# Performance work log

Hardware: AMD Instinct MI355X
Metric: run time of the kernel (lower is better)

The kernel has to match this reference:

```python
import jax, jax.numpy as jnp
import numpy as np

SH_C0 = 0.28209479177387814
SH_C1 = 0.4886025119029199
SH_C2 = (1.0925484305920792, -1.0925484305920792, 0.31539156525252005, -1.0925484305920792, 0.5462742152960396)
SH_C3 = (-0.5900435899266435, 2.890611442640554, -0.4570457994644658, 0.3731763325901154, -0.4570457994644658, 1.445305721320277, -0.5900435899266435)

BG = 128  # gaussians per compositing block


def quat_to_rot(q):
    # q: [N,4] normalized quaternion (w,x,y,z) -> [N,3,3]
    w, x, y, z = q[:, 0], q[:, 1], q[:, 2], q[:, 3]
    R = jnp.stack([
        1 - 2 * (y * y + z * z), 2 * (x * y - w * z), 2 * (x * z + w * y),
        2 * (x * y + w * z), 1 - 2 * (x * x + z * z), 2 * (y * z - w * x),
        2 * (x * z - w * y), 2 * (y * z + w * x), 1 - 2 * (x * x + y * y)],
        axis=-1)
    return R.reshape(-1, 3, 3)


def eval_sh(sh, d):
    # sh: [N,16,3] degree-3 SH coeffs; d: [N,3] unit view dirs -> [N,3] rgb
    x, y, z = d[:, 0:1], d[:, 1:2], d[:, 2:3]
    xx, yy, zz = x * x, y * y, z * z
    xy, yz, xz = x * y, y * z, x * z
    res = SH_C0 * sh[:, 0]
    res = res - SH_C1 * y * sh[:, 1] + SH_C1 * z * sh[:, 2] - SH_C1 * x * sh[:, 3]
    res = (res + SH_C2[0] * xy * sh[:, 4] + SH_C2[1] * yz * sh[:, 5]
           + SH_C2[2] * (2 * zz - xx - yy) * sh[:, 6]
           + SH_C2[3] * xz * sh[:, 7] + SH_C2[4] * (xx - yy) * sh[:, 8])
    res = (res + SH_C3[0] * y * (3 * xx - yy) * sh[:, 9] + SH_C3[1] * xy * z * sh[:, 10]
           + SH_C3[2] * y * (4 * zz - xx - yy) * sh[:, 11]
           + SH_C3[3] * z * (2 * zz - 3 * xx - 3 * yy) * sh[:, 12]
           + SH_C3[4] * x * (4 * zz - xx - yy) * sh[:, 13]
           + SH_C3[5] * z * (xx - yy) * sh[:, 14] + SH_C3[6] * x * (xx - 3 * yy) * sh[:, 15])
    return res


def gs_forward(pws, shs, alphas_raw, scales_raw, rots_raw, us, Rcw, tcw, intr, height, width):
    fx, fy, cx, cy = intr[0], intr[1], intr[2], intr[3]
    N = pws.shape[0]
    HW = height * width

    # activations (GSModel.forward)
    alphas = jax.nn.sigmoid(alphas_raw[:, 0])          # [N]
    scales = jnp.exp(scales_raw)                       # [N,3]
    rots = rots_raw / jnp.linalg.norm(rots_raw, axis=1, keepdims=True)

    # gsc.project
    pcs = pws @ Rcw.T + tcw                            # [N,3] camera frame
    depth = pcs[:, 2]
    zs = jnp.where(depth > 0.2, depth, 1.0)            # safe divide for culled pts
    u = jnp.stack([fx * pcs[:, 0] / zs + cx, fy * pcs[:, 1] / zs + cy], axis=-1)
    # the `us` input is a grad-capture dummy; forward value comes from projection
    u = u + us - jax.lax.stop_gradient(us)

    # gsc.computeCov3D: Cov3d = (R S)(R S)^T
    R = quat_to_rot(rots)
    M = R * scales[:, None, :]
    cov3d = M @ jnp.swapaxes(M, 1, 2)                  # [N,3,3]

    # gsc.computeCov2D: cov2d = J W Cov3d W^T J^T + 0.3 I
    tanfx = width / (2.0 * fx)
    tanfy = height / (2.0 * fy)
    tx = jnp.clip(pcs[:, 0] / zs, -1.3 * tanfx, 1.3 * tanfx) * zs
    ty = jnp.clip(pcs[:, 1] / zs, -1.3 * tanfy, 1.3 * tanfy) * zs
    zero = jnp.zeros_like(zs)
    J = jnp.stack([
        fx / zs, zero, -fx * tx / (zs * zs),
        zero, fy / zs, -fy * ty / (zs * zs)], axis=-1).reshape(N, 2, 3)
    T = jnp.einsum('nij,jk->nik', J, Rcw)              # [N,2,3]
    cov2d = jnp.einsum('nij,njk,nlk->nil', T, cov3d, T)
    cov2d = cov2d + 0.3 * jnp.eye(2, dtype=cov2d.dtype)
    a, b, c = cov2d[:, 0, 0], cov2d[:, 0, 1], cov2d[:, 1, 1]
    det = a * c - b * b
    valid = (depth > 0.2) & (det > 0)
    det_s = jnp.where(valid, det, 1.0)

    # gsc.inverseCov2D: conic + screen-space radius (areas)
    cinv = jnp.stack([c / det_s, -b / det_s, a / det_s], axis=-1)  # [N,3]
    mid = 0.5 * (a + c)
    lam = mid + jnp.sqrt(jnp.maximum(mid * mid - det, 0.1))
    radius = jnp.where(valid, jnp.ceil(3.0 * jnp.sqrt(lam)), 0.0)
    areas = jnp.stack([radius, radius], axis=-1)       # [N,2]

    # gsc.sh2Color
    twc = -Rcw.T @ tcw
    dirs = pws - twc
    dirs = dirs / jnp.linalg.norm(dirs, axis=1, keepdims=True)
    colors = jnp.maximum(eval_sh(shs.reshape(N, 16, 3), dirs) + 0.5, 0.0)  # [N,3]

    # gsc.splat: depth-sorted front-to-back alpha compositing over all pixels
    order = jnp.argsort(depth)
    nb = N // BG
    u_s = u[order].reshape(nb, BG, 2)
    cinv_s = cinv[order].reshape(nb, BG, 3)
    al_s = alphas[order].reshape(nb, BG)
    col_s = colors[order].reshape(nb, BG, 3)
    val_s = valid[order].reshape(nb, BG)

    ys, xs = jnp.meshgrid(jnp.arange(height, dtype=jnp.float32),
                          jnp.arange(width, dtype=jnp.float32), indexing='ij')
    px = xs.ravel()
    py = ys.ravel()

    @jax.checkpoint
    def body(carry, blk):
        logT, acc = carry                              # [HW], [3,HW]
        ub, cb, ab, colb, vb = blk
        dx = px[None, :] - ub[:, 0:1]                  # [BG,HW]
        dy = py[None, :] - ub[:, 1:2]
        power = -0.5 * (cb[:, 0:1] * dx * dx + cb[:, 2:3] * dy * dy) - cb[:, 1:2] * dx * dy
        alp = jnp.minimum(0.99, ab[:, None] * jnp.exp(power))
        alp = jnp.where((power <= 0) & (alp >= 1.0 / 255.0) & vb[:, None], alp, 0.0)
        l1m = jnp.log1p(-alp)
        cs = jnp.cumsum(l1m, axis=0)
        logT_i = logT[None, :] + jnp.concatenate(
            [jnp.zeros((1, HW), l1m.dtype), cs[:-1]], axis=0)  # exclusive transmittance
        Ti = jnp.exp(logT_i)
        w = jnp.where(Ti > 1e-4, alp * Ti, 0.0)        # early-termination at tau<1e-4
        acc = acc + jnp.einsum('gp,gc->cp', w, colb)
        return (logT + cs[-1], acc), None

    init = (jnp.zeros(HW, dtype=jnp.float32), jnp.zeros((3, HW), dtype=jnp.float32))
    (_, acc), _ = jax.lax.scan(body, init, (u_s, cinv_s, al_s, col_s, val_s))
    image = acc.reshape(3, height, width)
    return image, areas


def setup_inputs() -> dict:
    key = jax.random.key(0)
    ks = jax.random.split(key, 6)
    N, H, W = 8192, 256, 256
    pws = jax.random.normal(ks[0], (N, 3), jnp.float32) * 2.0 + jnp.array([0.0, 0.0, 6.0])
    shs = jax.random.normal(ks[1], (N, 48), jnp.float32) * 0.3
    alphas_raw = jax.random.normal(ks[2], (N, 1), jnp.float32)
    scales_raw = jax.random.normal(ks[3], (N, 3), jnp.float32) * 0.3 - 3.0
    rots_raw = jax.random.normal(ks[4], (N, 4), jnp.float32)
    us = jnp.zeros((N, 2), jnp.float32)
    Rcw = jnp.eye(3, dtype=jnp.float32)
    tcw = jnp.zeros((3,), jnp.float32)
    intr = jnp.array([400.0, 400.0, 128.0, 128.0], jnp.float32)  # fx, fy, cx, cy
    return {"pws": pws, "shs": shs, "alphas_raw": alphas_raw, "scales_raw": scales_raw,
            "rots_raw": rots_raw, "us": us, "Rcw": Rcw, "tcw": tcw, "intr": intr,
            "height": H, "width": W}


def reference(pws, shs, alphas_raw, scales_raw, rots_raw, us, Rcw, tcw, intr, height, width):
    return gs_forward(pws, shs, alphas_raw, scales_raw, rots_raw, us, Rcw, tcw, intr, height, width)
```

## Files before the change

kernel.cpp:

```cpp
#include <hip/hip_runtime.h>

__global__ __launch_bounds__(64) void k_pre(
    const float* __restrict__ pws, const float* __restrict__ shs,
    const float* __restrict__ alphas_raw, const float* __restrict__ scales_raw,
    const float* __restrict__ rots_raw, const float* __restrict__ Rcw,
    const float* __restrict__ tcw, const float* __restrict__ intr,
    int N, int W, int H, float* __restrict__ areas,
    unsigned long long* __restrict__ keys, unsigned* __restrict__ rank,
    float* __restrict__ P)
{
    int i = blockIdx.x * 64 + threadIdx.x;
    if (i >= N) return;
    rank[i] = 0u;

    float R00=Rcw[0],R01=Rcw[1],R02=Rcw[2];
    float R10=Rcw[3],R11=Rcw[4],R12=Rcw[5];
    float R20=Rcw[6],R21=Rcw[7],R22=Rcw[8];
    float t0=tcw[0],t1=tcw[1],t2=tcw[2];
    float fx=intr[0],fy=intr[1],cx=intr[2],cy=intr[3];

    float pwx=pws[i*3+0], pwy=pws[i*3+1], pwz=pws[i*3+2];
    float pcx = R00*pwx + R01*pwy + R02*pwz + t0;
    float pcy = R10*pwx + R11*pwy + R12*pwz + t1;
    float pcz = R20*pwx + R21*pwy + R22*pwz + t2;
    float depth = pcz;
    float zs = (depth > 0.2f) ? depth : 1.0f;
    float u0 = fx * pcx / zs + cx;
    float u1 = fy * pcy / zs + cy;

    float4 q4 = *reinterpret_cast<const float4*>(rots_raw + i*4);
    float qw=q4.x, qx=q4.y, qy=q4.z, qz=q4.w;
    float qn = sqrtf(qw*qw + qx*qx + qy*qy + qz*qz);
    qw/=qn; qx/=qn; qy/=qn; qz/=qn;
    float s0 = expf(scales_raw[i*3+0]);
    float s1 = expf(scales_raw[i*3+1]);
    float s2 = expf(scales_raw[i*3+2]);

    float xx=qx*qx, yy=qy*qy, zq=qz*qz;
    float xy=qx*qy, xz=qx*qz, yz=qy*qz;
    float wx=qw*qx, wy=qw*qy, wz=qw*qz;
    float r00=1.f-2.f*(yy+zq), r01=2.f*(xy-wz),     r02=2.f*(xz+wy);
    float r10=2.f*(xy+wz),     r11=1.f-2.f*(xx+zq), r12=2.f*(yz-wx);
    float r20=2.f*(xz-wy),     r21=2.f*(yz+wx),     r22=1.f-2.f*(xx+yy);

    float m00=r00*s0, m01=r01*s1, m02=r02*s2;
    float m10=r10*s0, m11=r11*s1, m12=r12*s2;
    float m20=r20*s0, m21=r21*s1, m22=r22*s2;
    float V00=m00*m00+m01*m01+m02*m02;
    float V01=m00*m10+m01*m11+m02*m12;
    float V02=m00*m20+m01*m21+m02*m22;
    float V11=m10*m10+m11*m11+m12*m12;
    float V12=m10*m20+m11*m21+m12*m22;
    float V22=m20*m20+m21*m21+m22*m22;

    float tanfx = (float)W / (2.f*fx), tanfy = (float)H / (2.f*fy);
    float limx = 1.3f*tanfx, limy = 1.3f*tanfy;
    float txl = fminf(fmaxf(pcx/zs, -limx), limx) * zs;
    float tyl = fminf(fmaxf(pcy/zs, -limy), limy) * zs;
    float iz = 1.f/zs, iz2 = iz*iz;
    float J00 = fx*iz, J02 = -fx*txl*iz2;
    float J11 = fy*iz, J12 = -fy*tyl*iz2;

    float T00=J00*R00+J02*R20, T01=J00*R01+J02*R21, T02=J00*R02+J02*R22;
    float T10=J11*R10+J12*R20, T11=J11*R11+J12*R21, T12=J11*R12+J12*R22;
    float A0=T00*V00+T01*V01+T02*V02;
    float A1=T00*V01+T01*V11+T02*V12;
    float A2=T00*V02+T01*V12+T02*V22;
    float B0=T10*V00+T11*V01+T12*V02;
    float B1=T10*V01+T11*V11+T12*V12;
    float B2=T10*V02+T11*V12+T12*V22;
    float ca = A0*T00+A1*T01+A2*T02 + 0.3f;
    float cb = A0*T10+A1*T11+A2*T12;
    float cc = B0*T10+B1*T11+B2*T12 + 0.3f;

    float det = ca*cc - cb*cb;
    bool valid = (depth > 0.2f) && (det > 0.f);
    float det_s = valid ? det : 1.f;
    float dinv = 1.f/det_s;
    float ci0 =  cc*dinv, ci1 = -cb*dinv, ci2 = ca*dinv;
    float mid = 0.5f*(ca+cc);
    float lam = mid + sqrtf(fmaxf(mid*mid - det, 0.1f));
    float radius = valid ? ceilf(3.f*sqrtf(lam)) : 0.f;
    areas[2*i+0] = radius;
    areas[2*i+1] = radius;

    float alpha = 1.f/(1.f + expf(-alphas_raw[i]));

    float tw0 = -(R00*t0 + R10*t1 + R20*t2);
    float tw1 = -(R01*t0 + R11*t1 + R21*t2);
    float tw2 = -(R02*t0 + R12*t1 + R22*t2);
    float dx_=pwx-tw0, dy_=pwy-tw1, dz_=pwz-tw2;
    float dn = sqrtf(dx_*dx_+dy_*dy_+dz_*dz_);
    float x=dx_/dn, y=dy_/dn, z=dz_/dn;
    float sxx=x*x, syy=y*y, szz=z*z;
    float sxy=x*y, syz=y*z, sxz=x*z;

    float shl[48];
    const float4* sh4 = reinterpret_cast<const float4*>(shs + i*48);
    #pragma unroll
    for (int k = 0; k < 12; ++k) {
        float4 v = sh4[k];
        shl[4*k+0]=v.x; shl[4*k+1]=v.y; shl[4*k+2]=v.z; shl[4*k+3]=v.w;
    }
    float col[3];
    #pragma unroll
    for (int c = 0; c < 3; ++c) {
        float res = 0.28209479177387814f*shl[0*3+c];
        res += -0.4886025119029199f*y*shl[1*3+c]
             +  0.4886025119029199f*z*shl[2*3+c]
             + -0.4886025119029199f*x*shl[3*3+c];
        res +=  1.0925484305920792f*sxy*shl[4*3+c]
             + -1.0925484305920792f*syz*shl[5*3+c]
             +  0.31539156525252005f*(2.f*szz-sxx-syy)*shl[6*3+c]
             + -1.0925484305920792f*sxz*shl[7*3+c]
             +  0.5462742152960396f*(sxx-syy)*shl[8*3+c];
        res += -0.5900435899266435f*y*(3.f*sxx-syy)*shl[9*3+c]
             +  2.890611442640554f*sxy*z*shl[10*3+c]
             + -0.4570457994644658f*y*(4.f*szz-sxx-syy)*shl[11*3+c]
             +  0.3731763325901154f*z*(2.f*szz-3.f*sxx-3.f*syy)*shl[12*3+c]
             + -0.4570457994644658f*x*(4.f*szz-sxx-syy)*shl[13*3+c]
             +  1.445305721320277f*z*(sxx-syy)*shl[14*3+c]
             + -0.5900435899266435f*x*(sxx-3.f*syy)*shl[15*3+c];
        col[c] = fmaxf(res + 0.5f, 0.f);
    }

    float rc2;
    if (!valid || 255.f*alpha < 0.999f) {
        rc2 = -1.f;
    } else {
        float r2 = 2.f*lam*logf(255.f*alpha);
        float r  = sqrtf(fmaxf(r2, 0.f)) + 1.f;
        rc2 = r*r;
    }

    P[0*N+i]=u0;  P[1*N+i]=u1;  P[2*N+i]=ci0; P[3*N+i]=ci1; P[4*N+i]=ci2;
    P[5*N+i]=alpha; P[6*N+i]=col[0]; P[7*N+i]=col[1]; P[8*N+i]=col[2];
    P[9*N+i]=rc2;

    unsigned ud = __float_as_uint(depth);
    ud = (ud & 0x80000000u) ? ~ud : (ud | 0x80000000u);
    keys[i] = ((unsigned long long)ud << 32) | (unsigned)i;
}

#define JC 512
__global__ __launch_bounds__(256) void k_rank_scatter(
    const unsigned long long* __restrict__ keys, int N,
    unsigned* __restrict__ rank, const float* __restrict__ Pun,
    float4* __restrict__ gA, float4* __restrict__ gB,
    float4* __restrict__ cull)
{
    __shared__ unsigned long long sk[JC];
    const int j0 = blockIdx.y * JC;
    const int nJ = gridDim.y;
    for (int t = threadIdx.x; t < JC; t += 256) {
        int j = j0 + t;
        sk[t] = (j < N) ? keys[j] : ~0ull;
    }
    __syncthreads();

    const int i = blockIdx.x * 256 + threadIdx.x;
    unsigned long long my = (i < N) ? keys[i] : 0ull;

    int c = 0;
    const ulonglong2* sk2 = (const ulonglong2*)sk;
    #pragma unroll 4
    for (int t = 0; t < JC/2; ++t) {
        ulonglong2 kk = sk2[t];
        c += (kk.x < my) ? 1 : 0;
        c += (kk.y < my) ? 1 : 0;
    }
    if (i < N) {
        unsigned old = atomicAdd(&rank[i], (unsigned)c + (1u << 20));
        if ((int)(old >> 20) == nJ - 1) {
            int s = (int)(old & 0xFFFFFu) + c;
            cull[s] = make_float4(Pun[0*N+i], Pun[1*N+i], Pun[9*N+i], 0.f);
            gA[s]   = make_float4(Pun[2*N+i], Pun[3*N+i], Pun[4*N+i], Pun[5*N+i]);
            gB[s]   = make_float4(Pun[6*N+i], Pun[7*N+i], Pun[8*N+i], 0.f);
        }
    }
}

__global__ __launch_bounds__(256, 8) void k_render(
    const float4* __restrict__ gA, const float4* __restrict__ gB,
    const float4* __restrict__ cull, int N, int W, int H,
    int nSuper, int superX, int tilesX, int tilesY, int nseg,
    float4* __restrict__ segbuf)
{
    const int tid  = threadIdx.x;
    const int wv   = tid >> 6, lane = tid & 63;
    const int sup  = blockIdx.x % nSuper, seg = blockIdx.x / nSuper;
    const int sX   = sup % superX, sY = sup / superX;
    const int tX   = (sX << 1) + (wv & 1);
    const int tY   = (sY << 1) + (wv >> 1);
    const bool tOK = (tX < tilesX) && (tY < tilesY);
    const int ix = (tX << 3) + (lane & 7);
    const int iy = (tY << 3) + (lane >> 3);
    const bool inb = tOK && (ix < W) && (iy < H);
    const float pxf = (float)ix, pyf = (float)iy;
    const float tx0 = (float)(tX << 3), ty0 = (float)(tY << 3);
    int tx1i = (tX << 3) + 7; if (tx1i > W-1) tx1i = W-1;
    int ty1i = (tY << 3) + 7; if (ty1i > H-1) ty1i = H-1;
    const float tx1 = (float)tx1i, ty1 = (float)ty1i;

    const int per = (N + nseg - 1) / nseg;
    const int g0 = seg * per;
    const int g1 = min(N, g0 + per);

    float T = inb ? 1.f : 0.f;
    float aR = 0.f, aG = 0.f, aB = 0.f;

    if (tOK) {
        int gl0 = min(g0 + lane, N - 1);
        float4 cu = cull[gl0];
        float4 a4 = gA[gl0];
        float4 b4 = gB[gl0];

        for (int base = g0; base < g1; base += 64) {
            float4 cu_n = make_float4(0.f, 0.f, -1.f, 0.f);
            float4 a4_n = make_float4(0.f, 0.f, 0.f, 0.f);
            float4 b4_n = make_float4(0.f, 0.f, 0.f, 0.f);
            if (base + 64 < g1) {
                int gln = min(base + 64 + lane, N - 1);
                cu_n = cull[gln];
                a4_n = gA[gln];
                b4_n = gB[gln];
            }

            int g = base + lane;
            bool ov = false;
            if (g < g1) {
                float cxp = fminf(fmaxf(cu.x, tx0), tx1);
                float cyp = fminf(fmaxf(cu.y, ty0), ty1);
                float ddx = cu.x - cxp, ddy = cu.y - cyp;
                ov = (ddx*ddx + ddy*ddy) <= cu.z;
            }

            unsigned long long mm = __ballot(ov);
            while (mm) {
                int l = __ffsll(mm) - 1;
                mm &= mm - 1ull;
                float su0 = __shfl(cu.x, l), su1 = __shfl(cu.y, l);
                float ci0 = __shfl(a4.x, l), ci1 = __shfl(a4.y, l);
                float ci2 = __shfl(a4.z, l), sal = __shfl(a4.w, l);
                float cr  = __shfl(b4.x, l), cg  = __shfl(b4.y, l);
                float cbv = __shfl(b4.z, l);
                float ddx = pxf - su0, ddy = pyf - su1;
                float power = -0.5f*(ci0*ddx*ddx + ci2*ddy*ddy) - ci1*ddx*ddy;
                float alp = fminf(0.99f, sal * __expf(power));
                alp = (power <= 0.f && alp >= (1.0f/255.0f)) ? alp : 0.f;
                float w = (T > 0.0001f) ? alp * T : 0.f;
                aR = fmaf(w, cr, aR);
                aG = fmaf(w, cg, aG);
                aB = fmaf(w, cbv, aB);
                T = T - T * alp;
            }
            if (__all(T <= 0.0001f)) break;
            cu = cu_n; a4 = a4_n; b4 = b4_n;
        }
    }

    if (inb) {
        int pix = iy * W + ix;
        segbuf[(size_t)seg * (size_t)(W*H) + pix] = make_float4(T, aR, aG, aB);
    }
}

__global__ __launch_bounds__(256) void k_combine(
    const float4* __restrict__ segbuf, int HW, int nseg,
    float* __restrict__ out)
{
    int p = blockIdx.x * 256 + threadIdx.x;
    if (p >= HW) return;
    float T = 1.f, r = 0.f, g = 0.f, b = 0.f;
    for (int s = 0; s < nseg; ++s) {
        float4 v = segbuf[(size_t)s * HW + p];
        r = fmaf(T, v.y, r);
        g = fmaf(T, v.z, g);
        b = fmaf(T, v.w, b);
        T *= v.x;
    }
    out[p] = r; out[HW + p] = g; out[2*HW + p] = b;
}

extern "C" void kernel_launch(void* const* d_in, const int* in_sizes, int n_in,
                              void* d_out, int out_size, void* d_ws, size_t ws_size,
                              hipStream_t stream) {
    const float* pws        = (const float*)d_in[0];
    const float* shs        = (const float*)d_in[1];
    const float* alphas_raw = (const float*)d_in[2];
    const float* scales_raw = (const float*)d_in[3];
    const float* rots_raw   = (const float*)d_in[4];
    const float* Rcw        = (const float*)d_in[6];
    const float* tcw        = (const float*)d_in[7];
    const float* intr       = (const float*)d_in[8];

    const int N  = in_sizes[0] / 3;
    const int HW = (out_size - 2 * N) / 3;
    int W = 1; while ((long long)W * W < (long long)HW) ++W;
    const int H = HW / W;

    float* out   = (float*)d_out;
    float* areas = out + 3 * HW;

    char* ws = (char*)d_ws;
    size_t off = 0;
    unsigned long long* keys = (unsigned long long*)(ws + off); off += (size_t)N * 8;
    unsigned* rank = (unsigned*)(ws + off);                     off += (size_t)N * 4;
    off = (off + 15) & ~(size_t)15;
    float* Pun = (float*)(ws + off);                            off += (size_t)10 * N * 4;
    off = (off + 15) & ~(size_t)15;
    float4* cullv = (float4*)(ws + off);                        off += (size_t)N * 16;
    float4* gA = (float4*)(ws + off);                           off += (size_t)N * 16;
    float4* gB = (float4*)(ws + off);                           off += (size_t)N * 16;
    float4* segbuf = (float4*)(ws + off);
    size_t remain = (ws_size > off) ? (ws_size - off) : 0;
    int nseg = 8;
    while (nseg > 1 && (size_t)nseg * (size_t)HW * 16 > remain) nseg >>= 1;

    k_pre<<<(N + 63) / 64, 64, 0, stream>>>(pws, shs, alphas_raw, scales_raw,
                                            rots_raw, Rcw, tcw, intr, N, W, H,
                                            areas, keys, rank, Pun);
    dim3 rgrid((N + 255) / 256, (N + JC - 1) / JC);
    k_rank_scatter<<<rgrid, 256, 0, stream>>>(keys, N, rank, Pun, gA, gB, cullv);
    int tilesX = (W + 7) / 8, tilesY = (H + 7) / 8;
    int superX = (tilesX + 1) / 2, superY = (tilesY + 1) / 2;
    int nSuper = superX * superY;
    k_render<<<nSuper * nseg, 256, 0, stream>>>(gA, gB, cullv, N, W, H,
                                                nSuper, superX, tilesX, tilesY,
                                                nseg, segbuf);
    k_combine<<<(HW + 255) / 256, 256, 0, stream>>>(segbuf, HW, nseg, out);
}
```

Measured before the change: 108.1 us.

## Build per-tile per-segment gaussian lists during scatter and render from them

The scatter kernel now bins each visible gaussian into per-(tile, depth-segment) lists of up to 64 entries using atomics. The render kernel switches to one 64-thread block per 8x8 tile, bitonic-sorts the short list by sorted index within the wave, and composites only the listed gaussians. When a list overflows it falls back to the old full-segment scan. The fallback now loads colour data only for overlapping gaussians and drops the prefetch. Costs are extra atomics in the scatter, a fixed nseg of 8 with no workspace-size check, and a serial per-gaussian bin loop in the scatter thread.

```diff
diff --git a/kernel.cpp b/kernel.cpp
--- a/kernel.cpp
+++ b/kernel.cpp
@@ -7,11 +7,12 @@
     const float* __restrict__ tcw, const float* __restrict__ intr,
     int N, int W, int H, float* __restrict__ areas,
     unsigned long long* __restrict__ keys, unsigned* __restrict__ rank,
-    float* __restrict__ P)
+    float* __restrict__ P, unsigned* __restrict__ cnts, int nCnt)
 {
     int i = blockIdx.x * 64 + threadIdx.x;
     if (i >= N) return;
     rank[i] = 0u;
+    for (int z = i; z < nCnt; z += N) cnts[z] = 0u;
 
     float R00=Rcw[0],R01=Rcw[1],R02=Rcw[2];
     float R10=Rcw[3],R11=Rcw[4],R12=Rcw[5];
@@ -143,11 +144,14 @@
 }
 
 #define JC 512
+#define BCAP 64
 __global__ __launch_bounds__(256) void k_rank_scatter(
     const unsigned long long* __restrict__ keys, int N,
     unsigned* __restrict__ rank, const float* __restrict__ Pun,
     float4* __restrict__ gA, float4* __restrict__ gB,
-    float4* __restrict__ cull)
+    float4* __restrict__ cull,
+    unsigned* __restrict__ cnts, int* __restrict__ list,
+    int tilesX, int tilesY, int nseg, int W, int H)
 {
     __shared__ unsigned long long sk[JC];
     const int j0 = blockIdx.y * JC;
@@ -173,68 +177,116 @@
         unsigned old = atomicAdd(&rank[i], (unsigned)c + (1u << 20));
         if ((int)(old >> 20) == nJ - 1) {
             int s = (int)(old & 0xFFFFFu) + c;
-            cull[s] = make_float4(Pun[0*N+i], Pun[1*N+i], Pun[9*N+i], 0.f);
+            float u0 = Pun[0*N+i], u1 = Pun[1*N+i], rc2 = Pun[9*N+i];
+            cull[s] = make_float4(u0, u1, rc2, 0.f);
             gA[s]   = make_float4(Pun[2*N+i], Pun[3*N+i], Pun[4*N+i], Pun[5*N+i]);
             gB[s]   = make_float4(Pun[6*N+i], Pun[7*N+i], Pun[8*N+i], 0.f);
+
+            if (rc2 > 0.f) {
+                const int per = (N + nseg - 1) / nseg;
+                const int seg = s / per;
+                float rr = sqrtf(rc2);
+                int x0 = (int)fminf(fmaxf(floorf((u0 - rr) * 0.125f), 0.f), (float)(tilesX - 1));
+                int x1 = (int)fminf(fmaxf(floorf((u0 + rr) * 0.125f), 0.f), (float)(tilesX - 1));
+                int y0 = (int)fminf(fmaxf(floorf((u1 - rr) * 0.125f), 0.f), (float)(tilesY - 1));
+                int y1 = (int)fminf(fmaxf(floorf((u1 + rr) * 0.125f), 0.f), (float)(tilesY - 1));
+                for (int ty = y0; ty <= y1; ++ty) {
+                    float by0 = (float)(ty << 3);
+                    float by1 = fminf(by0 + 7.f, (float)(H - 1));
+                    float cyp = fminf(fmaxf(u1, by0), by1);
+                    float ddy = u1 - cyp;
+                    for (int tx = x0; tx <= x1; ++tx) {
+                        float bx0 = (float)(tx << 3);
+                        float bx1 = fminf(bx0 + 7.f, (float)(W - 1));
+                        float cxp = fminf(fmaxf(u0, bx0), bx1);
+                        float ddx = u0 - cxp;
+                        if (ddx*ddx + ddy*ddy <= rc2) {
+                            int lid = (ty * tilesX + tx) * nseg + seg;
+                            unsigned pos = atomicAdd(&cnts[lid], 1u);
+                            if (pos < (unsigned)BCAP) list[lid * BCAP + (int)pos] = s;
+                        }
+                    }
+                }
+            }
         }
     }
 }
 
-__global__ __launch_bounds__(256, 8) void k_render(
+__global__ __launch_bounds__(64) void k_render(
     const float4* __restrict__ gA, const float4* __restrict__ gB,
-    const float4* __restrict__ cull, int N, int W, int H,
-    int nSuper, int superX, int tilesX, int tilesY, int nseg,
-    float4* __restrict__ segbuf)
+    const float4* __restrict__ cull, const unsigned* __restrict__ cnts,
+    const int* __restrict__ list, int N, int W, int H,
+    int nTiles, int nseg, float4* __restrict__ segbuf)
 {
-    const int tid  = threadIdx.x;
-    const int wv   = tid >> 6, lane = tid & 63;
-    const int sup  = blockIdx.x % nSuper, seg = blockIdx.x / nSuper;
-    const int sX   = sup % superX, sY = sup / superX;
-    const int tX   = (sX << 1) + (wv & 1);
-    const int tY   = (sY << 1) + (wv >> 1);
-    const bool tOK = (tX < tilesX) && (tY < tilesY);
+    const int lane = threadIdx.x;
+    const int tilesX = (W + 7) >> 3;
+    const int tile = blockIdx.x % nTiles, seg = blockIdx.x / nTiles;
+    const int tX = tile % tilesX, tY = tile / tilesX;
     const int ix = (tX << 3) + (lane & 7);
     const int iy = (tY << 3) + (lane >> 3);
-    const bool inb = tOK && (ix < W) && (iy < H);
+    const bool inb = (ix < W) && (iy < H);
     const float pxf = (float)ix, pyf = (float)iy;
-    const float tx0 = (float)(tX << 3), ty0 = (float)(tY << 3);
-    int tx1i = (tX << 3) + 7; if (tx1i > W-1) tx1i = W-1;
-    int ty1i = (tY << 3) + 7; if (ty1i > H-1) ty1i = H-1;
-    const float tx1 = (float)tx1i, ty1 = (float)ty1i;
-
-    const int per = (N + nseg - 1) / nseg;
-    const int g0 = seg * per;
-    const int g1 = min(N, g0 + per);
 
     float T = inb ? 1.f : 0.f;
     float aR = 0.f, aG = 0.f, aB = 0.f;
 
-    if (tOK) {
-        int gl0 = min(g0 + lane, N - 1);
-        float4 cu = cull[gl0];
-        float4 a4 = gA[gl0];
-        float4 b4 = gB[gl0];
-
+    const int lid = tile * nseg + seg;
+    int cnt = (int)cnts[lid];
+
+    if (cnt <= BCAP) {
+        int v = (lane < cnt) ? list[lid * BCAP + lane] : 0x7FFFFFFF;
+        #pragma unroll
+        for (int k = 2; k <= 64; k <<= 1) {
+            #pragma unroll
+            for (int j = k >> 1; j > 0; j >>= 1) {
+                int other = __shfl_xor(v, j);
+                bool up = ((lane & k) == 0);
+                bool takeMax = (((lane & j) != 0) == up);
+                v = takeMax ? max(v, other) : min(v, other);
+            }
+        }
+        float4 cu = make_float4(0.f,0.f,0.f,0.f);
+        float4 a4 = make_float4(0.f,0.f,0.f,0.f);
+        float4 b4 = make_float4(0.f,0.f,0.f,0.f);
+        if (lane < cnt) { cu = cull[v]; a4 = gA[v]; b4 = gB[v]; }
+        for (int e = 0; e < cnt; ++e) {
+            float su0 = __shfl(cu.x, e), su1 = __shfl(cu.y, e);
+            float ci0 = __shfl(a4.x, e), ci1 = __shfl(a4.y, e);
+            float ci2 = __shfl(a4.z, e), sal = __shfl(a4.w, e);
+            float cr  = __shfl(b4.x, e), cg  = __shfl(b4.y, e);
+            float cbv = __shfl(b4.z, e);
+            float ddx = pxf - su0, ddy = pyf - su1;
+            float power = -0.5f*(ci0*ddx*ddx + ci2*ddy*ddy) - ci1*ddx*ddy;
+            float alp = fminf(0.99f, sal * __expf(power));
+            alp = (power <= 0.f && alp >= (1.0f/255.0f)) ? alp : 0.f;
+            float w = (T > 0.0001f) ? alp * T : 0.f;
+            aR = fmaf(w, cr, aR);
+            aG = fmaf(w, cg, aG);
+            aB = fmaf(w, cbv, aB);
+            T = T - T * alp;
+        }
+    } else {
+        const float tx0 = (float)(tX << 3), ty0 = (float)(tY << 3);
+        int tx1i = (tX << 3) + 7; if (tx1i > W-1) tx1i = W-1;
+        int ty1i = (tY << 3) + 7; if (ty1i > H-1) ty1i = H-1;
+        const float tx1 = (float)tx1i, ty1 = (float)ty1i;
+        const int per = (N + nseg - 1) / nseg;
+        const int g0 = seg * per;
+        const int g1 = min(N, g0 + per);
         for (int base = g0; base < g1; base += 64) {
-            float4 cu_n = make_float4(0.f, 0.f, -1.f, 0.f);
-            float4 a4_n = make_float4(0.f, 0.f, 0.f, 0.f);
-            float4 b4_n = make_float4(0.f, 0.f, 0.f, 0.f);
-            if (base + 64 < g1) {
-                int gln = min(base + 64 + lane, N - 1);
-                cu_n = cull[gln];
-                a4_n = gA[gln];
-                b4_n = gB[gln];
-            }
-
             int g = base + lane;
             bool ov = false;
+            float4 cu = make_float4(0.f,0.f,0.f,0.f);
+            float4 a4 = make_float4(0.f,0.f,0.f,0.f);
+            float4 b4 = make_float4(0.f,0.f,0.f,0.f);
             if (g < g1) {
+                cu = cull[g];
                 float cxp = fminf(fmaxf(cu.x, tx0), tx1);
                 float cyp = fminf(fmaxf(cu.y, ty0), ty1);
                 float ddx = cu.x - cxp, ddy = cu.y - cyp;
                 ov = (ddx*ddx + ddy*ddy) <= cu.z;
+                if (ov) { a4 = gA[g]; b4 = gB[g]; }
             }
-
             unsigned long long mm = __ballot(ov);
             while (mm) {
                 int l = __ffsll(mm) - 1;
@@ -255,7 +307,6 @@
                 T = T - T * alp;
             }
             if (__all(T <= 0.0001f)) break;
-            cu = cu_n; a4 = a4_n; b4 = b4_n;
         }
     }
 
@@ -302,6 +353,11 @@
     float* out   = (float*)d_out;
     float* areas = out + 3 * HW;
 
+    const int nseg = 8;
+    int tilesX = (W + 7) / 8, tilesY = (H + 7) / 8;
+    int nTiles = tilesX * tilesY;
+    int nCnt = nTiles * nseg;
+
     char* ws = (char*)d_ws;
     size_t off = 0;
     unsigned long long* keys = (unsigned long long*)(ws + off); off += (size_t)N * 8;
@@ -312,21 +368,20 @@
     float4* cullv = (float4*)(ws + off);                        off += (size_t)N * 16;
     float4* gA = (float4*)(ws + off);                           off += (size_t)N * 16;
     float4* gB = (float4*)(ws + off);                           off += (size_t)N * 16;
+    unsigned* cnts = (unsigned*)(ws + off);                     off += (size_t)nCnt * 4;
+    off = (off + 15) & ~(size_t)15;
+    int* blist = (int*)(ws + off);                              off += (size_t)nCnt * BCAP * 4;
+    off = (off + 15) & ~(size_t)15;
     float4* segbuf = (float4*)(ws + off);
-    size_t remain = (ws_size > off) ? (ws_size - off) : 0;
-    int nseg = 8;
-    while (nseg > 1 && (size_t)nseg * (size_t)HW * 16 > remain) nseg >>= 1;
 
     k_pre<<<(N + 63) / 64, 64, 0, stream>>>(pws, shs, alphas_raw, scales_raw,
                                             rots_raw, Rcw, tcw, intr, N, W, H,
-                                            areas, keys, rank, Pun);
+                                            areas, keys, rank, Pun, cnts, nCnt);
     dim3 rgrid((N + 255) / 256, (N + JC - 1) / JC);
-    k_rank_scatter<<<rgrid, 256, 0, stream>>>(keys, N, rank, Pun, gA, gB, cullv);
-    int tilesX = (W + 7) / 8, tilesY = (H + 7) / 8;
-    int superX = (tilesX + 1) / 2, superY = (tilesY + 1) / 2;
-    int nSuper = superX * superY;
-    k_render<<<nSuper * nseg, 256, 0, stream>>>(gA, gB, cullv, N, W, H,
-                                                nSuper, superX, tilesX, tilesY,
-                                                nseg, segbuf);
+    k_rank_scatter<<<rgrid, 256, 0, stream>>>(keys, N, rank, Pun, gA, gB, cullv,
+                                              cnts, blist, tilesX, tilesY, nseg,
+                                              W, H);
+    k_render<<<nTiles * nseg, 64, 0, stream>>>(gA, gB, cullv, cnts, blist,
+                                               N, W, H, nTiles, nseg, segbuf);
     k_combine<<<(HW + 255) / 256, 256, 0, stream>>>(segbuf, HW, nseg, out);
 }
```

After: 408.7 us. +277.9%, slower.

## Render 16x16 tiles with four pixels per lane, one wave per block

Applied to the files above, without the earlier changes.

Each wave of the compositing kernel now covers a 16x16 tile, with every lane holding a 2x2 pixel quad. One ballot and one set of shuffles per gaussian is then shared across four pixels, which cuts cull-test and shuffle overhead per pixel. To keep enough blocks in flight, the gaussian list is split into 16 depth segments instead of 8. The trade-offs are a coarser cull test, since larger tiles admit more gaussians, weaker early termination because all four pixels must saturate, more register pressure, and a heavier combine pass.

```diff
diff --git a/kernel.cpp b/kernel.cpp
--- a/kernel.cpp
+++ b/kernel.cpp
@@ -180,88 +180,99 @@
     }
 }
 
-__global__ __launch_bounds__(256, 8) void k_render(
+__global__ __launch_bounds__(64) void k_render(
     const float4* __restrict__ gA, const float4* __restrict__ gB,
     const float4* __restrict__ cull, int N, int W, int H,
-    int nSuper, int superX, int tilesX, int tilesY, int nseg,
-    float4* __restrict__ segbuf)
+    int nTiles, int nseg, float4* __restrict__ segbuf)
 {
-    const int tid  = threadIdx.x;
-    const int wv   = tid >> 6, lane = tid & 63;
-    const int sup  = blockIdx.x % nSuper, seg = blockIdx.x / nSuper;
-    const int sX   = sup % superX, sY = sup / superX;
-    const int tX   = (sX << 1) + (wv & 1);
-    const int tY   = (sY << 1) + (wv >> 1);
-    const bool tOK = (tX < tilesX) && (tY < tilesY);
-    const int ix = (tX << 3) + (lane & 7);
-    const int iy = (tY << 3) + (lane >> 3);
-    const bool inb = tOK && (ix < W) && (iy < H);
-    const float pxf = (float)ix, pyf = (float)iy;
-    const float tx0 = (float)(tX << 3), ty0 = (float)(tY << 3);
-    int tx1i = (tX << 3) + 7; if (tx1i > W-1) tx1i = W-1;
-    int ty1i = (tY << 3) + 7; if (ty1i > H-1) ty1i = H-1;
+    const int lane = threadIdx.x;
+    const int tilesX = (W + 15) >> 4;
+    const int tile = blockIdx.x % nTiles, seg = blockIdx.x / nTiles;
+    const int tX = tile % tilesX, tY = tile / tilesX;
+    const int bx = (tX << 4) + ((lane & 7) << 1);
+    const int by = (tY << 4) + ((lane >> 3) << 1);
+
+    float pxs[4], pys[4];
+    bool  inb[4];
+    #pragma unroll
+    for (int q = 0; q < 4; ++q) {
+        int qx = bx + (q & 1), qy = by + (q >> 1);
+        pxs[q] = (float)qx; pys[q] = (float)qy;
+        inb[q] = (qx < W) && (qy < H);
+    }
+
+    const float tx0 = (float)(tX << 4), ty0 = (float)(tY << 4);
+    int tx1i = (tX << 4) + 15; if (tx1i > W-1) tx1i = W-1;
+    int ty1i = (tY << 4) + 15; if (ty1i > H-1) ty1i = H-1;
     const float tx1 = (float)tx1i, ty1 = (float)ty1i;
 
     const int per = (N + nseg - 1) / nseg;
     const int g0 = seg * per;
     const int g1 = min(N, g0 + per);
 
-    float T = inb ? 1.f : 0.f;
-    float aR = 0.f, aG = 0.f, aB = 0.f;
-
-    if (tOK) {
-        int gl0 = min(g0 + lane, N - 1);
-        float4 cu = cull[gl0];
-        float4 a4 = gA[gl0];
-        float4 b4 = gB[gl0];
-
-        for (int base = g0; base < g1; base += 64) {
-            float4 cu_n = make_float4(0.f, 0.f, -1.f, 0.f);
-            float4 a4_n = make_float4(0.f, 0.f, 0.f, 0.f);
-            float4 b4_n = make_float4(0.f, 0.f, 0.f, 0.f);
-            if (base + 64 < g1) {
-                int gln = min(base + 64 + lane, N - 1);
-                cu_n = cull[gln];
-                a4_n = gA[gln];
-                b4_n = gB[gln];
-            }
-
-            int g = base + lane;
-            bool ov = false;
-            if (g < g1) {
-                float cxp = fminf(fmaxf(cu.x, tx0), tx1);
-                float cyp = fminf(fmaxf(cu.y, ty0), ty1);
-                float ddx = cu.x - cxp, ddy = cu.y - cyp;
-                ov = (ddx*ddx + ddy*ddy) <= cu.z;
-            }
-
-            unsigned long long mm = __ballot(ov);
-            while (mm) {
-                int l = __ffsll(mm) - 1;
-                mm &= mm - 1ull;
-                float su0 = __shfl(cu.x, l), su1 = __shfl(cu.y, l);
-                float ci0 = __shfl(a4.x, l), ci1 = __shfl(a4.y, l);
-                float ci2 = __shfl(a4.z, l), sal = __shfl(a4.w, l);
-                float cr  = __shfl(b4.x, l), cg  = __shfl(b4.y, l);
-                float cbv = __shfl(b4.z, l);
-                float ddx = pxf - su0, ddy = pyf - su1;
+    float T[4], aR[4], aG[4], aB[4];
+    #pragma unroll
+    for (int q = 0; q < 4; ++q) { T[q] = inb[q] ? 1.f : 0.f; aR[q]=aG[q]=aB[q]=0.f; }
+
+    int gl0 = min(g0 + lane, N - 1);
+    float4 cu = cull[gl0];
+    float4 a4 = gA[gl0];
+    float4 b4 = gB[gl0];
+
+    for (int base = g0; base < g1; base += 64) {
+        float4 cu_n = make_float4(0.f, 0.f, -1.f, 0.f);
+        float4 a4_n = make_float4(0.f, 0.f, 0.f, 0.f);
+        float4 b4_n = make_float4(0.f, 0.f, 0.f, 0.f);
+        if (base + 64 < g1) {
+            int gln = min(base + 64 + lane, N - 1);
+            cu_n = cull[gln];
+            a4_n = gA[gln];
+            b4_n = gB[gln];
+        }
+
+        int g = base + lane;
+        bool ov = false;
+        if (g < g1) {
+            float cxp = fminf(fmaxf(cu.x, tx0), tx1);
+            float cyp = fminf(fmaxf(cu.y, ty0), ty1);
+            float ddx = cu.x - cxp, ddy = cu.y - cyp;
+            ov = (ddx*ddx + ddy*ddy) <= cu.z;
+        }
+
+        unsigned long long mm = __ballot(ov);
+        while (mm) {
+            int l = __ffsll(mm) - 1;
+            mm &= mm - 1ull;
+            float su0 = __shfl(cu.x, l), su1 = __shfl(cu.y, l);
+            float ci0 = __shfl(a4.x, l), ci1 = __shfl(a4.y, l);
+            float ci2 = __shfl(a4.z, l), sal = __shfl(a4.w, l);
+            float cr  = __shfl(b4.x, l), cg  = __shfl(b4.y, l);
+            float cbv = __shfl(b4.z, l);
+            #pragma unroll
+            for (int q = 0; q < 4; ++q) {
+                float ddx = pxs[q] - su0, ddy = pys[q] - su1;
                 float power = -0.5f*(ci0*ddx*ddx + ci2*ddy*ddy) - ci1*ddx*ddy;
                 float alp = fminf(0.99f, sal * __expf(power));
                 alp = (power <= 0.f && alp >= (1.0f/255.0f)) ? alp : 0.f;
-                float w = (T > 0.0001f) ? alp * T : 0.f;
-                aR = fmaf(w, cr, aR);
-                aG = fmaf(w, cg, aG);
-                aB = fmaf(w, cbv, aB);
-                T = T - T * alp;
+                float w = (T[q] > 0.0001f) ? alp * T[q] : 0.f;
+                aR[q] = fmaf(w, cr, aR[q]);
+                aG[q] = fmaf(w, cg, aG[q]);
+                aB[q] = fmaf(w, cbv, aB[q]);
+                T[q] = T[q] - T[q] * alp;
             }
-            if (__all(T <= 0.0001f)) break;
-            cu = cu_n; a4 = a4_n; b4 = b4_n;
-        }
-    }
-
-    if (inb) {
-        int pix = iy * W + ix;
-        segbuf[(size_t)seg * (size_t)(W*H) + pix] = make_float4(T, aR, aG, aB);
+        }
+        float Tm = fmaxf(fmaxf(T[0], T[1]), fmaxf(T[2], T[3]));
+        if (__all(Tm <= 0.0001f)) break;
+        cu = cu_n; a4 = a4_n; b4 = b4_n;
+    }
+
+    const size_t segBase = (size_t)seg * (size_t)(W * H);
+    #pragma unroll
+    for (int q = 0; q < 4; ++q) {
+        if (inb[q]) {
+            int pix = (by + (q >> 1)) * W + (bx + (q & 1));
+            segbuf[segBase + pix] = make_float4(T[q], aR[q], aG[q], aB[q]);
+        }
     }
 }
 
@@ -314,7 +325,7 @@
     float4* gB = (float4*)(ws + off);                           off += (size_t)N * 16;
     float4* segbuf = (float4*)(ws + off);
     size_t remain = (ws_size > off) ? (ws_size - off) : 0;
-    int nseg = 8;
+    int nseg = 16;
     while (nseg > 1 && (size_t)nseg * (size_t)HW * 16 > remain) nseg >>= 1;
 
     k_pre<<<(N + 63) / 64, 64, 0, stream>>>(pws, shs, alphas_raw, scales_raw,
@@ -322,11 +333,9 @@
                                             areas, keys, rank, Pun);
     dim3 rgrid((N + 255) / 256, (N + JC - 1) / JC);
     k_rank_scatter<<<rgrid, 256, 0, stream>>>(keys, N, rank, Pun, gA, gB, cullv);
-    int tilesX = (W + 7) / 8, tilesY = (H + 7) / 8;
-    int superX = (tilesX + 1) / 2, superY = (tilesY + 1) / 2;
-    int nSuper = superX * superY;
-    k_render<<<nSuper * nseg, 256, 0, stream>>>(gA, gB, cullv, N, W, H,
-                                                nSuper, superX, tilesX, tilesY,
-                                                nseg, segbuf);
+    int tilesX = (W + 15) / 16, tilesY = (H + 15) / 16;
+    int nTiles = tilesX * tilesY;
+    k_render<<<nTiles * nseg, 64, 0, stream>>>(gA, gB, cullv, N, W, H,
+                                               nTiles, nseg, segbuf);
     k_combine<<<(HW + 255) / 256, 256, 0, stream>>>(segbuf, HW, nseg, out);
 }
```

New measurement: 110.6 us. 2.3% more time.
